# Performance work log

Measured on AMD Instinct MI355X. Metric: run time of the kernel, lower is better.

## Reference

```python
import jax, jax.numpy as jnp
import numpy as np

DIM = 1024
N_HIDDEN = 64
NUM_HEADS = 16
B, S = 4, 1024
# original torch code: scale = sqrt(n_hidden // num_heads) = sqrt(64 // 16) = 2.0
SCALE = float(np.sqrt(N_HIDDEN // NUM_HEADS))


def setup_inputs() -> dict:
    key = jax.random.key(0)
    ks = jax.random.split(key, 10)
    lim = 1.0 / np.sqrt(DIM)          # nn.Linear default init range
    lim_o = 1.0 / np.sqrt(N_HIDDEN * NUM_HEADS)
    u = lambda k, shape, l: jax.random.uniform(k, shape, jnp.float32, -l, l)
    x = jax.random.normal(ks[0], (B, S, DIM), jnp.float32)
    attn_mask = jax.random.randint(ks[1], (B, S, S), 0, 2).astype(jnp.int32)
    # stacked per-head projection weights: [H, dim, n_hidden]
    Wq = u(ks[2], (NUM_HEADS, DIM, N_HIDDEN), lim)
    bq = u(ks[3], (NUM_HEADS, N_HIDDEN), lim)
    Wk = u(ks[4], (NUM_HEADS, DIM, N_HIDDEN), lim)
    bk = u(ks[5], (NUM_HEADS, N_HIDDEN), lim)
    Wv = u(ks[6], (NUM_HEADS, DIM, N_HIDDEN), lim)
    bv = u(ks[7], (NUM_HEADS, N_HIDDEN), lim)
    Wo = u(ks[8], (NUM_HEADS * N_HIDDEN, DIM), lim_o)
    bo = u(ks[9], (DIM,), lim_o)
    return {"x": x, "attn_mask": attn_mask, "Wq": Wq, "bq": bq,
            "Wk": Wk, "bk": bk, "Wv": Wv, "bv": bv, "Wo": Wo, "bo": bo}


def reference(x, attn_mask, Wq, bq, Wk, bk, Wv, bv, Wo, bo):
    # batched QKV across all heads (replaces the per-head Python loop)
    Q = jnp.einsum('bsd,hde->bhse', x, Wq) + bq[None, :, None, :]
    K = jnp.einsum('bsd,hde->bhse', x, Wk) + bk[None, :, None, :]
    V = jnp.einsum('bsd,hde->bhse', x, Wv) + bv[None, :, None, :]
    scores = jnp.einsum('bhse,bhte->bhst', Q, K) / SCALE
    alpha = jax.nn.softmax(scores, axis=-1)
    # faithful to original: zero out masked entries AFTER softmax, no renorm
    alpha = jnp.where(attn_mask[:, None, :, :] == 0, 0.0, alpha)  # [B,H,S,S]
    out = jnp.einsum('bhst,bhte->bhse', alpha, V)                 # [B,H,S,E]
    # torch.cat over heads on last dim == reshape to [B,S,H*E] in head order
    concat = out.transpose(0, 2, 1, 3).reshape(B, S, NUM_HEADS * N_HIDDEN)
    attn_output = concat @ Wo + bo                                # [B,S,dim]
    return attn_output, alpha
```

## Files before the change

kernel.cpp:

```cpp
#include <hip/hip_runtime.h>
#include <stdint.h>

#define S_LEN 1024
#define DIM   1024
#define NHID  64
#define NHEAD 16
#define NB    4

typedef __bf16 bf16x8 __attribute__((ext_vector_type(8)));
typedef float  f32x4  __attribute__((ext_vector_type(4)));
typedef unsigned short u16;

__device__ __forceinline__ u16 f2b(float f) {
  unsigned u = __float_as_uint(f);
  u += 0x7FFFu + ((u >> 16) & 1u);
  return (u16)(u >> 16);
}

__device__ __forceinline__ f32x4 mfma16(bf16x8 a, bf16x8 b, f32x4 c) {
  return __builtin_amdgcn_mfma_f32_16x16x32_bf16(a, b, c, 0, 0, 0);
}

__global__ __launch_bounds__(256) void k_cvt_x(const float* __restrict__ x,
                                               u16* __restrict__ xb) {
  int i = blockIdx.x * 256 + threadIdx.x;
  float4 v = ((const float4*)x)[i];
  ushort4 o;
  o.x = f2b(v.x); o.y = f2b(v.y); o.z = f2b(v.z); o.w = f2b(v.w);
  ((ushort4*)xb)[i] = o;
}

__global__ __launch_bounds__(256) void k_maskbits(const int* __restrict__ mask,
                                                  uint32_t* __restrict__ bits) {
  int w = blockIdx.x * 256 + threadIdx.x;
  const int4* mp = (const int4*)mask + (size_t)w * 8;
  uint32_t v = 0;
#pragma unroll
  for (int i = 0; i < 8; ++i) {
    int4 m = mp[i];
    v |= (m.x != 0 ? 1u : 0u) << (i * 4 + 0);
    v |= (m.y != 0 ? 1u : 0u) << (i * 4 + 1);
    v |= (m.z != 0 ? 1u : 0u) << (i * 4 + 2);
    v |= (m.w != 0 ? 1u : 0u) << (i * 4 + 3);
  }
  bits[w] = v;
}

__global__ __launch_bounds__(256) void k_transpose(const float* __restrict__ in,
                                                   u16* __restrict__ out,
                                                   int R, int C) {
  const float* ip = in + (size_t)blockIdx.x * R * C;
  u16* op = out + (size_t)blockIdx.x * R * C;
  __shared__ float tile[32][65];
  int r0 = blockIdx.y * 32, c0 = blockIdx.z * 64;
  int t = threadIdx.x;
  {
    int col = t & 63, rr = t >> 6;
#pragma unroll
    for (int p = 0; p < 8; ++p) {
      int r = p * 4 + rr;
      tile[r][col] = ip[(size_t)(r0 + r) * C + c0 + col];
    }
  }
  __syncthreads();
  {
    int d = t & 31, er = t >> 5;
#pragma unroll
    for (int p = 0; p < 8; ++p) {
      int e = p * 8 + er;
      op[(size_t)(c0 + e) * R + r0 + d] = f2b(tile[d][e]);
    }
  }
}

__global__ __launch_bounds__(256) void k_qkv(const u16* __restrict__ xb,
                                             const u16* __restrict__ Wtb,
                                             const float* __restrict__ bq,
                                             const float* __restrict__ bk,
                                             const float* __restrict__ bv,
                                             u16* __restrict__ Qb,
                                             u16* __restrict__ Kb,
                                             u16* __restrict__ Vtb) {
  __shared__ __align__(16) char lds[32768];
  int t = threadIdx.x, w = t >> 6, lane = t & 63;
  int l15 = lane & 15, l4 = lane >> 4;
  int m0 = blockIdx.x * 128, n0 = blockIdx.y * 128, sel = blockIdx.z;
  const u16* Wh = Wtb + (size_t)sel * (NHEAD * NHID * DIM);
  int wr = w >> 1, wc = w & 1;

  f32x4 acc[4][4];
  const f32x4 fz = {0.f, 0.f, 0.f, 0.f};
#pragma unroll
  for (int i = 0; i < 4; ++i)
#pragma unroll
    for (int j = 0; j < 4; ++j) acc[i][j] = fz;

  for (int kk = 0; kk < 16; ++kk) {
    int k0 = kk * 64;
#pragma unroll
    for (int c = 0; c < 4; ++c) {
      int idx = c * 256 + t, r = idx >> 3, cb = idx & 7;
      int4 v = *(const int4*)(xb + (size_t)(m0 + r) * DIM + k0 + cb * 8);
      *(int4*)(lds + r * 128 + ((cb * 16) ^ ((r & 7) << 4))) = v;
    }
#pragma unroll
    for (int c = 0; c < 4; ++c) {
      int idx = c * 256 + t, r = idx >> 3, cb = idx & 7;
      int4 v = *(const int4*)(Wh + (size_t)(n0 + r) * DIM + k0 + cb * 8);
      *(int4*)(lds + 16384 + r * 128 + ((cb * 16) ^ ((r & 7) << 4))) = v;
    }
    __syncthreads();
    bf16x8 a[4][2], bb[4][2];
#pragma unroll
    for (int mf = 0; mf < 4; ++mf)
#pragma unroll
      for (int kc = 0; kc < 2; ++kc) {
        int row = wr * 64 + mf * 16 + l15;
        int kb = kc * 64 + l4 * 16;
        a[mf][kc] = *(const bf16x8*)(lds + row * 128 + (kb ^ ((row & 7) << 4)));
      }
#pragma unroll
    for (int nf = 0; nf < 4; ++nf)
#pragma unroll
      for (int kc = 0; kc < 2; ++kc) {
        int row = wc * 64 + nf * 16 + l15;
        int kb = kc * 64 + l4 * 16;
        bb[nf][kc] = *(const bf16x8*)(lds + 16384 + row * 128 + (kb ^ ((row & 7) << 4)));
      }
#pragma unroll
    for (int kc = 0; kc < 2; ++kc)
#pragma unroll
      for (int mf = 0; mf < 4; ++mf)
#pragma unroll
        for (int nf = 0; nf < 4; ++nf)
          acc[mf][nf] = mfma16(a[mf][kc], bb[nf][kc], acc[mf][nf]);
    __syncthreads();
  }

  const float* bias = (sel == 0) ? bq : (sel == 1) ? bk : bv;
  float postScale = (sel == 0) ? 0.5f : 1.0f;
#pragma unroll
  for (int nf = 0; nf < 4; ++nf) {
    int n = n0 + wc * 64 + nf * 16 + l15;
    int h = n >> 6, e = n & 63;
    float bv_ = bias[n];
#pragma unroll
    for (int mf = 0; mf < 4; ++mf) {
      int mrow0 = m0 + wr * 64 + mf * 16 + l4 * 4;
      int b_ = mrow0 >> 10, s0 = mrow0 & 1023;
      if (sel == 2) {
        ushort4 pk;
        pk.x = f2b(acc[mf][nf][0] + bv_);
        pk.y = f2b(acc[mf][nf][1] + bv_);
        pk.z = f2b(acc[mf][nf][2] + bv_);
        pk.w = f2b(acc[mf][nf][3] + bv_);
        *(ushort4*)(Vtb + ((size_t)(b_ * NHEAD + h) * NHID + e) * S_LEN + s0) = pk;
      } else {
        u16* dst = (sel == 0) ? Qb : Kb;
#pragma unroll
        for (int j = 0; j < 4; ++j)
          dst[((size_t)(b_ * NHEAD + h) * S_LEN + s0 + j) * NHID + e] =
              f2b((acc[mf][nf][j] + bv_) * postScale);
      }
    }
  }
}

__global__ __launch_bounds__(256, 4) void k_attn(const u16* __restrict__ Qb,
                                                 const u16* __restrict__ Kb,
                                                 const u16* __restrict__ Vtb,
                                                 const uint32_t* __restrict__ mbitsG,
                                                 float* __restrict__ alphaOut,
                                                 u16* __restrict__ Ob) {
  __shared__ __align__(16) char smem[16896];
  float* redM = (float*)(smem + 16384);
  float* redS = (float*)(smem + 16640);
  char* chunkB = smem;
  int t = threadIdx.x, w = t >> 6, lane = t & 63;
  int l15 = lane & 15, l4 = lane >> 4;
  int q0 = blockIdx.x * 16;
  int bh = blockIdx.y, b = bh >> 4, hh = bh & 15;
  const u16* Qh = Qb + (size_t)bh * S_LEN * NHID;
  const u16* Kh = Kb + (size_t)bh * S_LEN * NHID;
  const u16* Vh = Vtb + (size_t)bh * NHID * S_LEN;
  int kbase = w * 256;

  const uint32_t* mrow = mbitsG + ((size_t)b * S_LEN + q0 + l15) * 32 + w * 8;
  uint4 mw0 = *(const uint4*)(mrow);
  uint4 mw1 = *(const uint4*)(mrow + 4);

  bf16x8 aq[2];
#pragma unroll
  for (int ec = 0; ec < 2; ++ec)
    aq[ec] = *(const bf16x8*)(Qh + (size_t)(q0 + l15) * NHID + ec * 32 + l4 * 8);

  f32x4 sc[16];
  const f32x4 fz = {0.f, 0.f, 0.f, 0.f};
#pragma unroll
  for (int kf = 0; kf < 16; ++kf) sc[kf] = fz;

#pragma unroll
  for (int kf = 0; kf < 16; ++kf) {
    int key = kbase + kf * 16 + l15;
    bf16x8 kb0 = *(const bf16x8*)(Kh + (size_t)key * NHID + l4 * 8);
    bf16x8 kb1 = *(const bf16x8*)(Kh + (size_t)key * NHID + 32 + l4 * 8);
    sc[kf] = mfma16(kb0, aq[0], sc[kf]);
    sc[kf] = mfma16(kb1, aq[1], sc[kf]);
  }

  float m;
  {
    f32x4 mm = sc[0];
#pragma unroll
    for (int kf = 1; kf < 16; ++kf) {
      mm[0] = fmaxf(mm[0], sc[kf][0]);
      mm[1] = fmaxf(mm[1], sc[kf][1]);
      mm[2] = fmaxf(mm[2], sc[kf][2]);
      mm[3] = fmaxf(mm[3], sc[kf][3]);
    }
    m = fmaxf(fmaxf(mm[0], mm[1]), fmaxf(mm[2], mm[3]));
  }
  m = fmaxf(m, __shfl_xor(m, 16));
  m = fmaxf(m, __shfl_xor(m, 32));
  if (lane < 16) redM[w * 16 + l15] = m;
  __syncthreads();
  float Mx = fmaxf(fmaxf(redM[l15], redM[16 + l15]),
                   fmaxf(redM[32 + l15], redM[48 + l15]));

  float s0 = 0.f, s1 = 0.f, s2 = 0.f, s3 = 0.f;
#pragma unroll
  for (int kf = 0; kf < 16; ++kf) {
    f32x4 p;
    p[0] = __expf(sc[kf][0] - Mx);
    p[1] = __expf(sc[kf][1] - Mx);
    p[2] = __expf(sc[kf][2] - Mx);
    p[3] = __expf(sc[kf][3] - Mx);
    sc[kf] = p;
    s0 += p[0]; s1 += p[1]; s2 += p[2]; s3 += p[3];
  }
  float ls = (s0 + s1) + (s2 + s3);
  ls += __shfl_xor(ls, 16);
  ls += __shfl_xor(ls, 32);
  if (lane < 16) redS[w * 16 + l15] = ls;
  __syncthreads();
  float inv = 1.f / (redS[l15] + redS[16 + l15] + redS[32 + l15] + redS[48 + l15]);

  float* abW = alphaOut + (size_t)bh * S_LEN * S_LEN;

  f32x4 o[4];
#pragma unroll
  for (int ef = 0; ef < 4; ++ef) o[ef] = fz;

  auto produce = [&](int c) {
    char* buf = chunkB + (w * 2 + (c & 1)) * 2048;
#pragma unroll
    for (int f = 0; f < 4; ++f) {
      int kf = c * 4 + f;
      int wi = kf >> 1;
      uint32_t mword;
      switch (wi) {
        case 0: mword = mw0.x; break;
        case 1: mword = mw0.y; break;
        case 2: mword = mw0.z; break;
        case 3: mword = mw0.w; break;
        case 4: mword = mw1.x; break;
        case 5: mword = mw1.y; break;
        case 6: mword = mw1.z; break;
        default: mword = mw1.w; break;
      }
      int bbase = ((kf & 1) << 4) + l4 * 4;
      f32x4 av;
      av[0] = ((mword >> (bbase + 0)) & 1u) ? sc[kf][0] * inv : 0.f;
      av[1] = ((mword >> (bbase + 1)) & 1u) ? sc[kf][1] * inv : 0.f;
      av[2] = ((mword >> (bbase + 2)) & 1u) ? sc[kf][2] * inv : 0.f;
      av[3] = ((mword >> (bbase + 3)) & 1u) ? sc[kf][3] * inv : 0.f;
      __builtin_nontemporal_store(
          av, (f32x4*)(abW + (size_t)(q0 + l15) * S_LEN + kbase + kf * 16 + l4 * 4));
      uint32_t p01 = (uint32_t)f2b(av[0]) | ((uint32_t)f2b(av[1]) << 16);
      uint32_t p23 = (uint32_t)f2b(av[2]) | ((uint32_t)f2b(av[3]) << 16);
      uint2 pk; pk.x = p01; pk.y = p23;
      *(uint2*)(buf + l15 * 128 + ((f * 32 + l4 * 8) ^ ((l15 & 7) << 4))) = pk;
    }
  };
  auto pv = [&](int c) {
    char* buf = chunkB + (w * 2 + (c & 1)) * 2048;
#pragma unroll
    for (int kc2 = 0; kc2 < 2; ++kc2) {
      int qrow = l15;
      bf16x8 pa = *(const bf16x8*)(buf + qrow * 128 +
                                   ((kc2 * 64 + l4 * 16) ^ ((qrow & 7) << 4)));
#pragma unroll
      for (int ef = 0; ef < 4; ++ef) {
        int e = ef * 16 + l15;
        bf16x8 vb = *(const bf16x8*)(Vh + (size_t)e * S_LEN + kbase + c * 64 +
                                     kc2 * 32 + l4 * 8);
        o[ef] = mfma16(pa, vb, o[ef]);
      }
    }
  };

  produce(0);
  produce(1); pv(0);
  produce(2); pv(1);
  produce(3); pv(2);
  pv(3);

  __syncthreads();
  float* redO = (float*)chunkB;
#pragma unroll
  for (int ef = 0; ef < 4; ++ef)
#pragma unroll
    for (int j = 0; j < 4; ++j)
      redO[w * 1024 + (l4 * 4 + j) * 64 + ef * 16 + l15] = o[ef][j];
  __syncthreads();
  {
    int e = t & 63, r4 = t >> 6;
#pragma unroll
    for (int p = 0; p < 4; ++p) {
      int r = p * 4 + r4;
      float s4 = redO[r * 64 + e] + redO[1024 + r * 64 + e] +
                 redO[2048 + r * 64 + e] + redO[3072 + r * 64 + e];
      Ob[(size_t)(b * S_LEN + q0 + r) * DIM + hh * NHID + e] = f2b(s4);
    }
  }
}

__global__ __launch_bounds__(256) void k_oproj(const u16* __restrict__ Ob,
                                               const u16* __restrict__ Wotb,
                                               const float* __restrict__ bo,
                                               float* __restrict__ out) {
  __shared__ __align__(16) char lds[32768];
  int t = threadIdx.x, w = t >> 6, lane = t & 63;
  int l15 = lane & 15, l4 = lane >> 4;
  int m0 = blockIdx.x * 128, n0 = blockIdx.y * 128;
  int wr = w >> 1, wc = w & 1;
  f32x4 acc[4][4];
  const f32x4 fz = {0.f, 0.f, 0.f, 0.f};
#pragma unroll
  for (int i = 0; i < 4; ++i)
#pragma unroll
    for (int j = 0; j < 4; ++j) acc[i][j] = fz;

  for (int kk = 0; kk < 16; ++kk) {
    int k0 = kk * 64;
#pragma unroll
    for (int c = 0; c < 4; ++c) {
      int idx = c * 256 + t, r = idx >> 3, cb = idx & 7;
      int4 v = *(const int4*)(Ob + (size_t)(m0 + r) * DIM + k0 + cb * 8);
      *(int4*)(lds + r * 128 + ((cb * 16) ^ ((r & 7) << 4))) = v;
    }
#pragma unroll
    for (int c = 0; c < 4; ++c) {
      int idx = c * 256 + t, r = idx >> 3, cb = idx & 7;
      int4 v = *(const int4*)(Wotb + (size_t)(n0 + r) * DIM + k0 + cb * 8);
      *(int4*)(lds + 16384 + r * 128 + ((cb * 16) ^ ((r & 7) << 4))) = v;
    }
    __syncthreads();
    bf16x8 a[4][2], bb[4][2];
#pragma unroll
    for (int mf = 0; mf < 4; ++mf)
#pragma unroll
      for (int kc = 0; kc < 2; ++kc) {
        int row = wr * 64 + mf * 16 + l15;
        int kb = kc * 64 + l4 * 16;
        a[mf][kc] = *(const bf16x8*)(lds + row * 128 + (kb ^ ((row & 7) << 4)));
      }
#pragma unroll
    for (int nf = 0; nf < 4; ++nf)
#pragma unroll
      for (int kc = 0; kc < 2; ++kc) {
        int row = wc * 64 + nf * 16 + l15;
        int kb = kc * 64 + l4 * 16;
        bb[nf][kc] = *(const bf16x8*)(lds + 16384 + row * 128 + (kb ^ ((row & 7) << 4)));
      }
#pragma unroll
    for (int kc = 0; kc < 2; ++kc)
#pragma unroll
      for (int mf = 0; mf < 4; ++mf)
#pragma unroll
        for (int nf = 0; nf < 4; ++nf)
          acc[mf][nf] = mfma16(a[mf][kc], bb[nf][kc], acc[mf][nf]);
    __syncthreads();
  }
#pragma unroll
  for (int nf = 0; nf < 4; ++nf) {
    int n = n0 + wc * 64 + nf * 16 + l15;
    float bv_ = bo[n];
#pragma unroll
    for (int mf = 0; mf < 4; ++mf)
#pragma unroll
      for (int j = 0; j < 4; ++j) {
        int m = m0 + wr * 64 + mf * 16 + l4 * 4 + j;
        out[(size_t)m * DIM + n] = acc[mf][nf][j] + bv_;
      }
  }
}

extern "C" void kernel_launch(void* const* d_in, const int* in_sizes, int n_in,
                              void* d_out, int out_size, void* d_ws, size_t ws_size,
                              hipStream_t stream) {
  const float* x    = (const float*)d_in[0];
  const int*   mask = (const int*)d_in[1];
  const float* Wq   = (const float*)d_in[2];
  const float* bq   = (const float*)d_in[3];
  const float* Wk   = (const float*)d_in[4];
  const float* bk   = (const float*)d_in[5];
  const float* Wv   = (const float*)d_in[6];
  const float* bv   = (const float*)d_in[7];
  const float* Wo   = (const float*)d_in[8];
  const float* bo   = (const float*)d_in[9];
  float* out = (float*)d_out;
  float* alphaOut = out + (size_t)NB * S_LEN * DIM;

  char* ws = (char*)d_ws;
  u16* xb    = (u16*)(ws);
  u16* Wtb   = (u16*)(ws + 8388608);
  u16* Wotb  = (u16*)(ws + 14680064);
  u16* Qb    = (u16*)(ws + 16777216);
  u16* Kb    = (u16*)(ws + 25165824);
  u16* Vtb   = (u16*)(ws + 33554432);
  u16* Ob    = (u16*)(ws + 41943040);
  uint32_t* mbits = (uint32_t*)(ws + 50331648);

  k_maskbits<<<512, 256, 0, stream>>>(mask, mbits);
  k_cvt_x<<<4096, 256, 0, stream>>>(x, xb);
  k_transpose<<<dim3(16, 32, 1), 256, 0, stream>>>(Wq, Wtb,           1024, 64);
  k_transpose<<<dim3(16, 32, 1), 256, 0, stream>>>(Wk, Wtb + 1048576, 1024, 64);
  k_transpose<<<dim3(16, 32, 1), 256, 0, stream>>>(Wv, Wtb + 2097152, 1024, 64);
  k_transpose<<<dim3(1, 32, 16), 256, 0, stream>>>(Wo, Wotb,          1024, 1024);
  k_qkv<<<dim3(32, 8, 3), 256, 0, stream>>>(xb, Wtb, bq, bk, bv, Qb, Kb, Vtb);
  k_attn<<<dim3(64, 64), 256, 0, stream>>>(Qb, Kb, Vtb, mbits, alphaOut, Ob);
  k_oproj<<<dim3(32, 8), 256, 0, stream>>>(Ob, Wotb, bo, out);
}
```

Measured before the change: 242.5 us.

## Give each attention wave full key range with two-pass recomputed scores

```diff
diff --git a/kernel.cpp b/kernel.cpp
--- a/kernel.cpp
+++ b/kernel.cpp
@@ -166,116 +166,75 @@
   }
 }
 
-__global__ __launch_bounds__(256, 4) void k_attn(const u16* __restrict__ Qb,
-                                                 const u16* __restrict__ Kb,
-                                                 const u16* __restrict__ Vtb,
-                                                 const uint32_t* __restrict__ mbitsG,
-                                                 float* __restrict__ alphaOut,
-                                                 u16* __restrict__ Ob) {
-  __shared__ __align__(16) char smem[16896];
-  float* redM = (float*)(smem + 16384);
-  float* redS = (float*)(smem + 16640);
-  char* chunkB = smem;
+__global__ __launch_bounds__(256) void k_attn(const u16* __restrict__ Qb,
+                                              const u16* __restrict__ Kb,
+                                              const u16* __restrict__ Vtb,
+                                              const uint32_t* __restrict__ mbitsG,
+                                              float* __restrict__ alphaOut,
+                                              u16* __restrict__ Ob) {
+  __shared__ __align__(16) char smem[16384];
   int t = threadIdx.x, w = t >> 6, lane = t & 63;
   int l15 = lane & 15, l4 = lane >> 4;
-  int q0 = blockIdx.x * 16;
+  int q0 = blockIdx.x * 64 + w * 16;
   int bh = blockIdx.y, b = bh >> 4, hh = bh & 15;
   const u16* Qh = Qb + (size_t)bh * S_LEN * NHID;
   const u16* Kh = Kb + (size_t)bh * S_LEN * NHID;
   const u16* Vh = Vtb + (size_t)bh * NHID * S_LEN;
-  int kbase = w * 256;
-
-  const uint32_t* mrow = mbitsG + ((size_t)b * S_LEN + q0 + l15) * 32 + w * 8;
-  uint4 mw0 = *(const uint4*)(mrow);
-  uint4 mw1 = *(const uint4*)(mrow + 4);
+  char* myB = smem + w * 4096;
 
   bf16x8 aq[2];
 #pragma unroll
   for (int ec = 0; ec < 2; ++ec)
     aq[ec] = *(const bf16x8*)(Qh + (size_t)(q0 + l15) * NHID + ec * 32 + l4 * 8);
 
-  f32x4 sc[16];
   const f32x4 fz = {0.f, 0.f, 0.f, 0.f};
-#pragma unroll
-  for (int kf = 0; kf < 16; ++kf) sc[kf] = fz;
-
-#pragma unroll
-  for (int kf = 0; kf < 16; ++kf) {
-    int key = kbase + kf * 16 + l15;
+
+  float s0 = 0.f, s1 = 0.f, s2 = 0.f, s3 = 0.f;
+#pragma unroll 4
+  for (int kf = 0; kf < 64; ++kf) {
+    int key = kf * 16 + l15;
     bf16x8 kb0 = *(const bf16x8*)(Kh + (size_t)key * NHID + l4 * 8);
     bf16x8 kb1 = *(const bf16x8*)(Kh + (size_t)key * NHID + 32 + l4 * 8);
-    sc[kf] = mfma16(kb0, aq[0], sc[kf]);
-    sc[kf] = mfma16(kb1, aq[1], sc[kf]);
-  }
-
-  float m;
-  {
-    f32x4 mm = sc[0];
-#pragma unroll
-    for (int kf = 1; kf < 16; ++kf) {
-      mm[0] = fmaxf(mm[0], sc[kf][0]);
-      mm[1] = fmaxf(mm[1], sc[kf][1]);
-      mm[2] = fmaxf(mm[2], sc[kf][2]);
-      mm[3] = fmaxf(mm[3], sc[kf][3]);
-    }
-    m = fmaxf(fmaxf(mm[0], mm[1]), fmaxf(mm[2], mm[3]));
-  }
-  m = fmaxf(m, __shfl_xor(m, 16));
-  m = fmaxf(m, __shfl_xor(m, 32));
-  if (lane < 16) redM[w * 16 + l15] = m;
-  __syncthreads();
-  float Mx = fmaxf(fmaxf(redM[l15], redM[16 + l15]),
-                   fmaxf(redM[32 + l15], redM[48 + l15]));
-
-  float s0 = 0.f, s1 = 0.f, s2 = 0.f, s3 = 0.f;
-#pragma unroll
-  for (int kf = 0; kf < 16; ++kf) {
-    f32x4 p;
-    p[0] = __expf(sc[kf][0] - Mx);
-    p[1] = __expf(sc[kf][1] - Mx);
-    p[2] = __expf(sc[kf][2] - Mx);
-    p[3] = __expf(sc[kf][3] - Mx);
-    sc[kf] = p;
-    s0 += p[0]; s1 += p[1]; s2 += p[2]; s3 += p[3];
+    f32x4 sct = fz;
+    sct = mfma16(kb0, aq[0], sct);
+    sct = mfma16(kb1, aq[1], sct);
+    s0 += __expf(sct[0]);
+    s1 += __expf(sct[1]);
+    s2 += __expf(sct[2]);
+    s3 += __expf(sct[3]);
   }
   float ls = (s0 + s1) + (s2 + s3);
   ls += __shfl_xor(ls, 16);
   ls += __shfl_xor(ls, 32);
-  if (lane < 16) redS[w * 16 + l15] = ls;
-  __syncthreads();
-  float inv = 1.f / (redS[l15] + redS[16 + l15] + redS[32 + l15] + redS[48 + l15]);
+  float inv = 1.f / ls;
 
   float* abW = alphaOut + (size_t)bh * S_LEN * S_LEN;
+  const uint32_t* mrowP = mbitsG + ((size_t)b * S_LEN + q0 + l15) * 32;
 
   f32x4 o[4];
 #pragma unroll
   for (int ef = 0; ef < 4; ++ef) o[ef] = fz;
 
   auto produce = [&](int c) {
-    char* buf = chunkB + (w * 2 + (c & 1)) * 2048;
+    char* buf = myB + (c & 1) * 2048;
+    uint2 mw = *(const uint2*)(mrowP + c * 2);
 #pragma unroll
     for (int f = 0; f < 4; ++f) {
-      int kf = c * 4 + f;
-      int wi = kf >> 1;
-      uint32_t mword;
-      switch (wi) {
-        case 0: mword = mw0.x; break;
-        case 1: mword = mw0.y; break;
-        case 2: mword = mw0.z; break;
-        case 3: mword = mw0.w; break;
-        case 4: mword = mw1.x; break;
-        case 5: mword = mw1.y; break;
-        case 6: mword = mw1.z; break;
-        default: mword = mw1.w; break;
-      }
-      int bbase = ((kf & 1) << 4) + l4 * 4;
+      int key = c * 64 + f * 16 + l15;
+      bf16x8 kb0 = *(const bf16x8*)(Kh + (size_t)key * NHID + l4 * 8);
+      bf16x8 kb1 = *(const bf16x8*)(Kh + (size_t)key * NHID + 32 + l4 * 8);
+      f32x4 sct = fz;
+      sct = mfma16(kb0, aq[0], sct);
+      sct = mfma16(kb1, aq[1], sct);
+      uint32_t mword = (f & 2) ? mw.y : mw.x;
+      int bbase = ((f & 1) << 4) + l4 * 4;
       f32x4 av;
-      av[0] = ((mword >> (bbase + 0)) & 1u) ? sc[kf][0] * inv : 0.f;
-      av[1] = ((mword >> (bbase + 1)) & 1u) ? sc[kf][1] * inv : 0.f;
-      av[2] = ((mword >> (bbase + 2)) & 1u) ? sc[kf][2] * inv : 0.f;
-      av[3] = ((mword >> (bbase + 3)) & 1u) ? sc[kf][3] * inv : 0.f;
+      av[0] = ((mword >> (bbase + 0)) & 1u) ? __expf(sct[0]) * inv : 0.f;
+      av[1] = ((mword >> (bbase + 1)) & 1u) ? __expf(sct[1]) * inv : 0.f;
+      av[2] = ((mword >> (bbase + 2)) & 1u) ? __expf(sct[2]) * inv : 0.f;
+      av[3] = ((mword >> (bbase + 3)) & 1u) ? __expf(sct[3]) * inv : 0.f;
       __builtin_nontemporal_store(
-          av, (f32x4*)(abW + (size_t)(q0 + l15) * S_LEN + kbase + kf * 16 + l4 * 4));
+          av, (f32x4*)(abW + (size_t)(q0 + l15) * S_LEN + c * 64 + f * 16 + l4 * 4));
       uint32_t p01 = (uint32_t)f2b(av[0]) | ((uint32_t)f2b(av[1]) << 16);
       uint32_t p23 = (uint32_t)f2b(av[2]) | ((uint32_t)f2b(av[3]) << 16);
       uint2 pk; pk.x = p01; pk.y = p23;
@@ -283,16 +242,15 @@
     }
   };
   auto pv = [&](int c) {
-    char* buf = chunkB + (w * 2 + (c & 1)) * 2048;
+    char* buf = myB + (c & 1) * 2048;
 #pragma unroll
     for (int kc2 = 0; kc2 < 2; ++kc2) {
-      int qrow = l15;
-      bf16x8 pa = *(const bf16x8*)(buf + qrow * 128 +
-                                   ((kc2 * 64 + l4 * 16) ^ ((qrow & 7) << 4)));
+      bf16x8 pa = *(const bf16x8*)(buf + l15 * 128 +
+                                   ((kc2 * 64 + l4 * 16) ^ ((l15 & 7) << 4)));
 #pragma unroll
       for (int ef = 0; ef < 4; ++ef) {
         int e = ef * 16 + l15;
-        bf16x8 vb = *(const bf16x8*)(Vh + (size_t)e * S_LEN + kbase + c * 64 +
+        bf16x8 vb = *(const bf16x8*)(Vh + (size_t)e * S_LEN + c * 64 +
                                      kc2 * 32 + l4 * 8);
         o[ef] = mfma16(pa, vb, o[ef]);
       }
@@ -300,29 +258,15 @@
   };
 
   produce(0);
-  produce(1); pv(0);
-  produce(2); pv(1);
-  produce(3); pv(2);
-  pv(3);
-
-  __syncthreads();
-  float* redO = (float*)chunkB;
+  for (int c = 1; c < 16; ++c) { produce(c); pv(c - 1); }
+  pv(15);
+
 #pragma unroll
   for (int ef = 0; ef < 4; ++ef)
 #pragma unroll
     for (int j = 0; j < 4; ++j)
-      redO[w * 1024 + (l4 * 4 + j) * 64 + ef * 16 + l15] = o[ef][j];
-  __syncthreads();
-  {
-    int e = t & 63, r4 = t >> 6;
-#pragma unroll
-    for (int p = 0; p < 4; ++p) {
-      int r = p * 4 + r4;
-      float s4 = redO[r * 64 + e] + redO[1024 + r * 64 + e] +
-                 redO[2048 + r * 64 + e] + redO[3072 + r * 64 + e];
-      Ob[(size_t)(b * S_LEN + q0 + r) * DIM + hh * NHID + e] = f2b(s4);
-    }
-  }
+      Ob[(size_t)(b * S_LEN + q0 + l4 * 4 + j) * DIM + hh * NHID + ef * 16 + l15] =
+          f2b(o[ef][j]);
 }
 
 __global__ __launch_bounds__(256) void k_oproj(const u16* __restrict__ Ob,
@@ -429,6 +373,6 @@
   k_transpose<<<dim3(16, 32, 1), 256, 0, stream>>>(Wv, Wtb + 2097152, 1024, 64);
   k_transpose<<<dim3(1, 32, 16), 256, 0, stream>>>(Wo, Wotb,          1024, 1024);
   k_qkv<<<dim3(32, 8, 3), 256, 0, stream>>>(xb, Wtb, bq, bk, bv, Qb, Kb, Vtb);
-  k_attn<<<dim3(64, 64), 256, 0, stream>>>(Qb, Kb, Vtb, mbits, alphaOut, Ob);
+  k_attn<<<dim3(16, 64), 256, 0, stream>>>(Qb, Kb, Vtb, mbits, alphaOut, Ob);
   k_oproj<<<dim3(32, 8), 256, 0, stream>>>(Ob, Wotb, bo, out);
 }
```

Result: slower. 284.1 us (+17.2%).
